# Kernel optimization log

Measured on AMD Instinct MI355X. Metric: run time of the kernel, lower is better.

## Reference

```python
import jax, jax.numpy as jnp
import numpy as np

B, K, C, NCLS = 4096, 20, 512, 8631


def setup_inputs() -> dict:
    key = jax.random.key(0)
    k0, k1, k2, k3 = jax.random.split(key, 4)
    x = jax.random.normal(k0, (B * K, C), dtype=jnp.float32)
    # NAN pooling (torch.cat of [1,C,K] tensors) requires uniform set lengths
    lst_lens = jnp.full((B,), K, dtype=jnp.int32)
    # learned params (torch init zeros them out, which degenerates the math to
    # mean pooling; use small random values for a meaningful correctness baseline)
    q = jax.random.normal(k1, (C,), dtype=jnp.float32) * 0.02        # NAN_Attention.q
    W_att = jax.random.normal(k2, (C, C), dtype=jnp.float32) * 0.02  # attention fc
    b_att = jnp.zeros((C,), dtype=jnp.float32)
    W_fc = jax.random.normal(k3, (NCLS, C), dtype=jnp.float32) * 0.02  # classifier
    b_fc = jnp.zeros((NCLS,), dtype=jnp.float32)
    return {"x": x, "lst_lens": lst_lens, "q": q, "W_att": W_att,
            "b_att": b_att, "W_fc": W_fc, "b_fc": b_fc}


def reference(x, lst_lens, q, W_att, b_att, W_fc, b_fc):
    eps = 1e-12
    # F.normalize: L2 normalize each row
    xn = x / jnp.maximum(jnp.linalg.norm(x, axis=1, keepdims=True), eps)
    nset = lst_lens.shape[0]
    k = xn.shape[0] // nset              # uniform set length (required by NAN cat)
    xs = xn.reshape(nset, k, -1)         # [B, K, C]  (== Xs.transpose of [B,C,K])

    # pass 1: global query q -> attention-weighted mean r
    s1 = jax.nn.softmax(jnp.einsum('c,bkc->bk', q, xs), axis=-1)   # [B, K]
    r = jnp.einsum('bk,bkc->bc', s1, xs)                            # [B, C]

    # pass 2: adapted query new_q = tanh(fc(r))
    new_q = jnp.tanh(r @ W_att.T + b_att)                           # [B, C]
    s2 = jax.nn.softmax(jnp.einsum('bc,bkc->bk', new_q, xs), axis=-1)
    feats = jnp.einsum('bk,bkc->bc', s2, xs)                        # [B, C]

    logits = feats @ W_fc.T + b_fc                                  # [B, NCLS]
    return feats, logits
```

## Files before the change

kernel.cpp:

```cpp
#include <hip/hip_runtime.h>
#include <math.h>

#define BB   4096
#define KK   20
#define CC   512
#define NCLS 8631
#define NPAD 8704
#define KSP  1536

typedef __attribute__((ext_vector_type(8))) short bf16x8;
typedef __attribute__((ext_vector_type(4))) float f32x4;

static __device__ __forceinline__ unsigned short f2bf(float f) {
    unsigned int u = __float_as_uint(f);
    u += 0x7FFFu + ((u >> 16) & 1u);
    return (unsigned short)(u >> 16);
}
static __device__ __forceinline__ float bf2f(unsigned short h) {
    return __uint_as_float(((unsigned int)h) << 16);
}

__global__ __launch_bounds__(320) void pool_kernel(
    const float* __restrict__ x,
    const float* __restrict__ qbase, size_t q_stride,
    float* __restrict__ outv)
{
    __shared__ float xs[KK][CC];
    __shared__ float red[KK];
    __shared__ float dots[KK];

    const int b   = blockIdx.x;
    const int tid = threadIdx.x;

    const float4* src = (const float4*)(x + (size_t)b * (KK * CC));
    float4* dst = (float4*)&xs[0][0];
    #pragma unroll
    for (int i = tid; i < KK * CC / 4; i += 320) dst[i] = src[i];

    const float* qv = qbase + (size_t)b * q_stride;
    __syncthreads();

    const int g = tid >> 4;
    const int l = tid & 15;
    float ss = 0.f, qd = 0.f;
    for (int c = l; c < CC; c += 16) {
        float v = xs[g][c];
        ss = fmaf(v, v, ss);
        qd = fmaf(qv[c], v, qd);
    }
    #pragma unroll
    for (int m = 8; m >= 1; m >>= 1) {
        ss += __shfl_xor(ss, m);
        qd += __shfl_xor(qd, m);
    }
    if (l == 0) {
        float inv = 1.f / fmaxf(sqrtf(ss), 1e-12f);
        red[g]  = inv;
        dots[g] = qd * inv;
    }
    __syncthreads();

    if (tid < KK) {
        float m = -1e30f;
        #pragma unroll
        for (int k = 0; k < KK; ++k) m = fmaxf(m, dots[k]);
        float s = 0.f;
        #pragma unroll
        for (int k = 0; k < KK; ++k) s += __expf(dots[k] - m);
        float w = __expf(dots[tid] - m) / s;
        red[tid] = w * red[tid];
    }
    __syncthreads();

    float* ob = outv + (size_t)b * CC;
    for (int c = tid; c < CC; c += 320) {
        float acc = 0.f;
        #pragma unroll
        for (int k = 0; k < KK; ++k) acc = fmaf(red[k], xs[k][c], acc);
        ob[c] = acc;
    }
}

template<int BM, int BN, int BK, int TM, int TN, bool TANH>
__global__ __launch_bounds__(256) void gemm_bt(
    const float* __restrict__ A,
    const float* __restrict__ Bt,
    const float* __restrict__ bias,
    float* __restrict__ Cmat,
    int M, int N, int Kd)
{
    constexpr int NT = (BM / TM) * (BN / TN);
    static_assert(NT == 256, "256 threads expected");
    static_assert(BM * BK == NT * 4 && BN * BK == NT * 4, "one float4 per thread per tile");

    __shared__ float As[BK][BM];
    __shared__ float Bs[BK][BN];

    const int tid = threadIdx.x;
    const int m0 = blockIdx.x * BM;
    const int n0 = blockIdx.y * BN;
    constexpr int TX = BN / TN;
    const int tx = tid % TX;
    const int ty = tid / TX;

    constexpr int KV = BK / 4;
    const int lr = tid / KV;
    const int lc = (tid % KV) * 4;

    float acc[TM][TN] = {};

    for (int k0 = 0; k0 < Kd; k0 += BK) {
        float4 av = *(const float4*)&A[(size_t)(m0 + lr) * Kd + k0 + lc];
        float4 bv = make_float4(0.f, 0.f, 0.f, 0.f);
        int nrow = n0 + lr;
        if (nrow < N) bv = *(const float4*)&Bt[(size_t)nrow * Kd + k0 + lc];

        __syncthreads();
        As[lc + 0][lr] = av.x; As[lc + 1][lr] = av.y;
        As[lc + 2][lr] = av.z; As[lc + 3][lr] = av.w;
        Bs[lc + 0][lr] = bv.x; Bs[lc + 1][lr] = bv.y;
        Bs[lc + 2][lr] = bv.z; Bs[lc + 3][lr] = bv.w;
        __syncthreads();

        #pragma unroll
        for (int kk = 0; kk < BK; ++kk) {
            float a[TM], bb[TN];
            #pragma unroll
            for (int u = 0; u < TM; u += 4)
                *(float4*)&a[u] = *(const float4*)&As[kk][ty * TM + u];
            #pragma unroll
            for (int u = 0; u < TN; u += 4)
                *(float4*)&bb[u] = *(const float4*)&Bs[kk][tx * TN + u];
            #pragma unroll
            for (int i = 0; i < TM; ++i)
                #pragma unroll
                for (int j = 0; j < TN; ++j)
                    acc[i][j] = fmaf(a[i], bb[j], acc[i][j]);
        }
    }

    #pragma unroll
    for (int i = 0; i < TM; ++i) {
        int m = m0 + ty * TM + i;
        #pragma unroll
        for (int j = 0; j < TN; ++j) {
            int n = n0 + tx * TN + j;
            if (n < N) {
                float v = acc[i][j] + bias[n];
                if (TANH) v = tanhf(v);
                Cmat[(size_t)m * N + n] = v;
            }
        }
    }
}

template<int L0, int L1, int L2>
__global__ __launch_bounds__(256) void conv_split(
    const float* __restrict__ in, unsigned short* __restrict__ out,
    int rows_in, int rows_out)
{
    int idx = blockIdx.x * 256 + threadIdx.x;
    int row = idx >> 7;
    if (row >= rows_out) return;
    int c4 = (idx & 127) << 2;

    float4 v = make_float4(0.f, 0.f, 0.f, 0.f);
    if (row < rows_in) v = *(const float4*)&in[(size_t)row * CC + c4];

    unsigned short h0 = f2bf(v.x), h1 = f2bf(v.y), h2 = f2bf(v.z), h3 = f2bf(v.w);
    ushort4 hv = make_ushort4(h0, h1, h2, h3);
    ushort4 lv = make_ushort4(f2bf(v.x - bf2f(h0)), f2bf(v.y - bf2f(h1)),
                              f2bf(v.z - bf2f(h2)), f2bf(v.w - bf2f(h3)));

    unsigned short* o = out + (size_t)row * KSP + c4;
    *(ushort4*)(o)          = L0 ? lv : hv;
    *(ushort4*)(o + CC)     = L1 ? lv : hv;
    *(ushort4*)(o + 2 * CC) = L2 ? lv : hv;
}

__global__ __launch_bounds__(256) void gemm_mfma_bt(
    const unsigned short* __restrict__ A,
    const unsigned short* __restrict__ B,
    const float* __restrict__ bias,
    float* __restrict__ Cmat,
    int Nn)
{
    __shared__ unsigned short As[128][32];
    __shared__ unsigned short Bs[128][32];

    const int tid  = threadIdx.x;
    const int lane = tid & 63;
    const int w    = tid >> 6;
    const int m0   = blockIdx.x * 128;
    const int n0   = blockIdx.y * 128;
    const int wr   = w >> 1;
    const int wc   = w & 1;

    f32x4 acc[4][4] = {};

    const int chunk0 = w * 128;

    for (int k0 = 0; k0 < KSP; k0 += 32) {
        __syncthreads();
        #pragma unroll
        for (int j = 0; j < 2; ++j) {
            const int cbase = chunk0 + j * 64;
            const int ch    = cbase + lane;
            const int row   = ch >> 2;
            const int kcol  = (ch & 3) << 3;
            const unsigned short* ga = A + (size_t)(m0 + row) * KSP + k0 + kcol;
            __builtin_amdgcn_global_load_lds(
                (const __attribute__((address_space(1))) void*)ga,
                (__attribute__((address_space(3))) void*)((char*)&As[0][0] + cbase * 16),
                16, 0, 0);
            const unsigned short* gb = B + (size_t)(n0 + row) * KSP + k0 + kcol;
            __builtin_amdgcn_global_load_lds(
                (const __attribute__((address_space(1))) void*)gb,
                (__attribute__((address_space(3))) void*)((char*)&Bs[0][0] + cbase * 16),
                16, 0, 0);
        }
        __syncthreads();

        const int kk = (lane >> 4) << 3;
        const int rl = lane & 15;
        bf16x8 af[4], bfr[4];
        #pragma unroll
        for (int i = 0; i < 4; ++i)
            af[i] = *(const bf16x8*)&As[wr * 64 + i * 16 + rl][kk];
        #pragma unroll
        for (int j = 0; j < 4; ++j)
            bfr[j] = *(const bf16x8*)&Bs[wc * 64 + j * 16 + rl][kk];

        #pragma unroll
        for (int i = 0; i < 4; ++i)
            #pragma unroll
            for (int j = 0; j < 4; ++j)
                acc[i][j] = __builtin_amdgcn_mfma_f32_16x16x32_bf16(
                    af[i], bfr[j], acc[i][j], 0, 0, 0);
    }

    const int rowb = m0 + wr * 64 + ((lane >> 4) << 2);
    const int colb = n0 + wc * 64 + (lane & 15);
    #pragma unroll
    for (int j = 0; j < 4; ++j) {
        const int n = colb + j * 16;
        if (n < Nn) {
            const float bia = bias[n];
            #pragma unroll
            for (int i = 0; i < 4; ++i) {
                #pragma unroll
                for (int r = 0; r < 4; ++r) {
                    const int m = rowb + i * 16 + r;
                    Cmat[(size_t)m * Nn + n] = acc[i][j][r] + bia;
                }
            }
        }
    }
}

extern "C" void kernel_launch(void* const* d_in, const int* in_sizes, int n_in,
                              void* d_out, int out_size, void* d_ws, size_t ws_size,
                              hipStream_t stream)
{
    const float* x     = (const float*)d_in[0];
    const float* q     = (const float*)d_in[2];
    const float* W_att = (const float*)d_in[3];
    const float* b_att = (const float*)d_in[4];
    const float* W_fc  = (const float*)d_in[5];
    const float* b_fc  = (const float*)d_in[6];

    float* feats  = (float*)d_out;
    float* logits = feats + (size_t)BB * CC;

    float* r_buf  = logits;
    float* nq_buf = logits + (size_t)BB * CC;

    const size_t needA = (size_t)BB * KSP * sizeof(unsigned short);
    const size_t needB = (size_t)NPAD * KSP * sizeof(unsigned short);
    const bool use_mfma = ws_size >= needA + needB;
    unsigned short* Abuf = (unsigned short*)d_ws;
    unsigned short* Bbuf = Abuf + (size_t)BB * KSP;

    pool_kernel<<<BB, 320, 0, stream>>>(x, q, (size_t)0, r_buf);

    gemm_bt<64, 64, 16, 4, 4, true><<<dim3(BB / 64, CC / 64), 256, 0, stream>>>(
        r_buf, W_att, b_att, nq_buf, BB, CC, CC);

    pool_kernel<<<BB, 320, 0, stream>>>(x, nq_buf, (size_t)CC, feats);

    if (use_mfma) {
        conv_split<0, 0, 1><<<(NPAD * (CC / 4)) / 256, 256, 0, stream>>>(
            W_fc, Bbuf, NCLS, NPAD);
        conv_split<0, 1, 0><<<(BB * (CC / 4)) / 256, 256, 0, stream>>>(
            feats, Abuf, BB, BB);
        gemm_mfma_bt<<<dim3(BB / 128, NPAD / 128), 256, 0, stream>>>(
            Abuf, Bbuf, b_fc, logits, NCLS);
    } else {
        gemm_bt<128, 128, 8, 8, 8, false><<<dim3(BB / 128, (NCLS + 127) / 128), 256, 0, stream>>>(
            feats, W_fc, b_fc, logits, BB, NCLS, CC);
    }
}
```

Measured before the change: 654.4 us.

## Add 256x256 pipelined MFMA classifier GEMM, MFMA attention GEMM, vectorized pooling

Replaces the 128x128 classifier GEMM with a 256x256-tile, 512-thread kernel that uses a 4-slot LDS ring fed by direct global-to-LDS loads, a swizzled LDS layout, XCD-aware block remapping and setprio around the MFMA bursts. The attention fc GEMM moves from the FP32 SIMT kernel to the split-bf16 MFMA path with tanh fused into its epilogue, which adds conversion kernels and workspace. The pooling kernel is vectorized to float4 LDS reads and stores. Together these target the large classifier GEMM and the scalar attention GEMM, at the cost of more workspace, high LDS use per block, and a more complex synchronization scheme.

```diff
diff --git a/kernel.cpp b/kernel.cpp
--- a/kernel.cpp
+++ b/kernel.cpp
@@ -7,6 +7,7 @@
 #define NCLS 8631
 #define NPAD 8704
 #define KSP  1536
+#define NTK  48
 
 typedef __attribute__((ext_vector_type(8))) short bf16x8;
 typedef __attribute__((ext_vector_type(4))) float f32x4;
@@ -34,7 +35,6 @@
 
     const float4* src = (const float4*)(x + (size_t)b * (KK * CC));
     float4* dst = (float4*)&xs[0][0];
-    #pragma unroll
     for (int i = tid; i < KK * CC / 4; i += 320) dst[i] = src[i];
 
     const float* qv = qbase + (size_t)b * q_stride;
@@ -43,10 +43,14 @@
     const int g = tid >> 4;
     const int l = tid & 15;
     float ss = 0.f, qd = 0.f;
-    for (int c = l; c < CC; c += 16) {
-        float v = xs[g][c];
-        ss = fmaf(v, v, ss);
-        qd = fmaf(qv[c], v, qd);
+    #pragma unroll
+    for (int c = 0; c < CC; c += 64) {
+        float4 v  = *(const float4*)&xs[g][c + l * 4];
+        float4 q4 = *(const float4*)&qv[c + l * 4];
+        ss = fmaf(v.x, v.x, ss); ss = fmaf(v.y, v.y, ss);
+        ss = fmaf(v.z, v.z, ss); ss = fmaf(v.w, v.w, ss);
+        qd = fmaf(q4.x, v.x, qd); qd = fmaf(q4.y, v.y, qd);
+        qd = fmaf(q4.z, v.z, qd); qd = fmaf(q4.w, v.w, qd);
     }
     #pragma unroll
     for (int m = 8; m >= 1; m >>= 1) {
@@ -73,11 +77,16 @@
     __syncthreads();
 
     float* ob = outv + (size_t)b * CC;
-    for (int c = tid; c < CC; c += 320) {
-        float acc = 0.f;
-        #pragma unroll
-        for (int k = 0; k < KK; ++k) acc = fmaf(red[k], xs[k][c], acc);
-        ob[c] = acc;
+    for (int c = tid * 4; c < CC; c += 1280) {
+        float4 a = make_float4(0.f, 0.f, 0.f, 0.f);
+        #pragma unroll
+        for (int k = 0; k < KK; ++k) {
+            float w = red[k];
+            float4 v = *(const float4*)&xs[k][c];
+            a.x = fmaf(w, v.x, a.x); a.y = fmaf(w, v.y, a.y);
+            a.z = fmaf(w, v.z, a.z); a.w = fmaf(w, v.w, a.w);
+        }
+        *(float4*)&ob[c] = a;
     }
 }
 
@@ -91,8 +100,6 @@
 {
     constexpr int NT = (BM / TM) * (BN / TN);
     static_assert(NT == 256, "256 threads expected");
-    static_assert(BM * BK == NT * 4 && BN * BK == NT * 4, "one float4 per thread per tile");
-
     __shared__ float As[BK][BM];
     __shared__ float Bs[BK][BN];
 
@@ -102,7 +109,6 @@
     constexpr int TX = BN / TN;
     const int tx = tid % TX;
     const int ty = tid / TX;
-
     constexpr int KV = BK / 4;
     const int lr = tid / KV;
     const int lc = (tid % KV) * 4;
@@ -114,14 +120,12 @@
         float4 bv = make_float4(0.f, 0.f, 0.f, 0.f);
         int nrow = n0 + lr;
         if (nrow < N) bv = *(const float4*)&Bt[(size_t)nrow * Kd + k0 + lc];
-
         __syncthreads();
         As[lc + 0][lr] = av.x; As[lc + 1][lr] = av.y;
         As[lc + 2][lr] = av.z; As[lc + 3][lr] = av.w;
         Bs[lc + 0][lr] = bv.x; Bs[lc + 1][lr] = bv.y;
         Bs[lc + 2][lr] = bv.z; Bs[lc + 3][lr] = bv.w;
         __syncthreads();
-
         #pragma unroll
         for (int kk = 0; kk < BK; ++kk) {
             float a[TM], bb[TN];
@@ -138,7 +142,6 @@
                     acc[i][j] = fmaf(a[i], bb[j], acc[i][j]);
         }
     }
-
     #pragma unroll
     for (int i = 0; i < TM; ++i) {
         int m = m0 + ty * TM + i;
@@ -178,6 +181,7 @@
     *(ushort4*)(o + 2 * CC) = L2 ? lv : hv;
 }
 
+template<bool TANH>
 __global__ __launch_bounds__(256) void gemm_mfma_bt(
     const unsigned short* __restrict__ A,
     const unsigned short* __restrict__ B,
@@ -197,7 +201,6 @@
     const int wc   = w & 1;
 
     f32x4 acc[4][4] = {};
-
     const int chunk0 = w * 128;
 
     for (int k0 = 0; k0 < KSP; k0 += 32) {
@@ -251,11 +254,142 @@
                 #pragma unroll
                 for (int r = 0; r < 4; ++r) {
                     const int m = rowb + i * 16 + r;
-                    Cmat[(size_t)m * Nn + n] = acc[i][j][r] + bia;
+                    float v = acc[i][j][r] + bia;
+                    if (TANH) v = tanhf(v);
+                    Cmat[(size_t)m * Nn + n] = v;
                 }
             }
         }
     }
+}
+
+__global__ __launch_bounds__(512, 2) void gemm_mfma256(
+    const unsigned short* __restrict__ A,
+    const unsigned short* __restrict__ B,
+    const float* __restrict__ bias,
+    float* __restrict__ Cmat,
+    int Nn, int mblocks)
+{
+    __shared__ char smem[131072];
+
+    const int tid  = threadIdx.x;
+    const int lane = tid & 63;
+    const int w    = tid >> 6;
+    const int wm   = w >> 2;
+    const int wn   = w & 3;
+    const int rl   = lane & 15;
+    const int cw   = lane >> 4;
+
+    const int cpx = (int)gridDim.x >> 3;
+    const int wg  = ((int)blockIdx.x & 7) * cpx + ((int)blockIdx.x >> 3);
+    const int m0  = (wg % mblocks) * 256;
+    const int n0  = (wg / mblocks) * 256;
+
+    const int rowA = tid >> 2;
+    const int lcs  = (tid & 3) ^ ((rowA >> 1) & 3);
+    const unsigned short* pA0 = A + (size_t)(m0 + rowA) * KSP + lcs * 8;
+    const unsigned short* pA1 = pA0 + (size_t)128 * KSP;
+    const unsigned short* pB0 = B + (size_t)(n0 + rowA) * KSP + lcs * 8;
+    const unsigned short* pB1 = pB0 + (size_t)128 * KSP;
+    const int wbyte = w * 1024;
+
+    #define STAGE_A(slot, k0s)                                                  \
+        do {                                                                    \
+            __builtin_amdgcn_global_load_lds(                                   \
+                (const __attribute__((address_space(1))) void*)(pA0 + (k0s)),   \
+                (__attribute__((address_space(3))) void*)(smem + (slot) * 16384 + wbyte), \
+                16, 0, 0);                                                      \
+            __builtin_amdgcn_global_load_lds(                                   \
+                (const __attribute__((address_space(1))) void*)(pA1 + (k0s)),   \
+                (__attribute__((address_space(3))) void*)(smem + (slot) * 16384 + 8192 + wbyte), \
+                16, 0, 0);                                                      \
+        } while (0)
+    #define STAGE_B(slot, k0s)                                                  \
+        do {                                                                    \
+            __builtin_amdgcn_global_load_lds(                                   \
+                (const __attribute__((address_space(1))) void*)(pB0 + (k0s)),   \
+                (__attribute__((address_space(3))) void*)(smem + 65536 + (slot) * 16384 + wbyte), \
+                16, 0, 0);                                                      \
+            __builtin_amdgcn_global_load_lds(                                   \
+                (const __attribute__((address_space(1))) void*)(pB1 + (k0s)),   \
+                (__attribute__((address_space(3))) void*)(smem + 65536 + (slot) * 16384 + 8192 + wbyte), \
+                16, 0, 0);                                                      \
+        } while (0)
+
+    const int albase = rl * 64 + ((cw ^ ((rl >> 1) & 3)) << 4);
+
+    f32x4 acc[8][4] = {};
+
+    #pragma unroll
+    for (int pt = 0; pt < 3; ++pt) {
+        STAGE_A(pt, pt * 32);
+        STAGE_B(pt, pt * 32);
+    }
+    asm volatile("s_waitcnt vmcnt(8)" ::: "memory");
+    __builtin_amdgcn_s_barrier();
+
+    for (int t = 0; t < NTK; ++t) {
+        const int slot = t & 3;
+        const int ts   = t + 3;
+        const int k0s  = (ts < NTK) ? ts * 32 : 0;
+        const int sst  = ts & 3;
+        const char* sa = smem + slot * 16384 + wm * 8192 + albase;
+        const char* sb = smem + 65536 + slot * 16384 + wn * 4096 + albase;
+
+        bf16x8 af[4], bf[4];
+        #pragma unroll
+        for (int i = 0; i < 4; ++i) af[i] = *(const bf16x8*)(sa + i * 1024);
+        #pragma unroll
+        for (int n = 0; n < 4; ++n) bf[n] = *(const bf16x8*)(sb + n * 1024);
+        STAGE_A(sst, k0s);
+        __builtin_amdgcn_s_barrier();
+        asm volatile("s_waitcnt lgkmcnt(0)" ::: "memory");
+        __builtin_amdgcn_s_setprio(1);
+        #pragma unroll
+        for (int i = 0; i < 4; ++i)
+            #pragma unroll
+            for (int n = 0; n < 4; ++n)
+                acc[i][n] = __builtin_amdgcn_mfma_f32_16x16x32_bf16(
+                    af[i], bf[n], acc[i][n], 0, 0, 0);
+        __builtin_amdgcn_s_setprio(0);
+        __builtin_amdgcn_s_barrier();
+
+        #pragma unroll
+        for (int i = 0; i < 4; ++i) af[i] = *(const bf16x8*)(sa + 4096 + i * 1024);
+        STAGE_B(sst, k0s);
+        __builtin_amdgcn_s_barrier();
+        asm volatile("s_waitcnt lgkmcnt(0)" ::: "memory");
+        __builtin_amdgcn_s_setprio(1);
+        #pragma unroll
+        for (int i = 0; i < 4; ++i)
+            #pragma unroll
+            for (int n = 0; n < 4; ++n)
+                acc[4 + i][n] = __builtin_amdgcn_mfma_f32_16x16x32_bf16(
+                    af[i], bf[n], acc[4 + i][n], 0, 0, 0);
+        __builtin_amdgcn_s_setprio(0);
+        asm volatile("s_waitcnt vmcnt(8)" ::: "memory");
+        __builtin_amdgcn_s_barrier();
+    }
+    asm volatile("s_waitcnt vmcnt(0)" ::: "memory");
+
+    const int mwb = m0 + wm * 128 + (cw << 2);
+    const int nwb = n0 + wn * 64 + rl;
+    #pragma unroll
+    for (int mf = 0; mf < 8; ++mf) {
+        #pragma unroll
+        for (int n = 0; n < 4; ++n) {
+            const int ncol = nwb + n * 16;
+            if (ncol < Nn) {
+                const float bia = bias[ncol];
+                float* cp = Cmat + (size_t)(mwb + mf * 16) * Nn + ncol;
+                #pragma unroll
+                for (int r = 0; r < 4; ++r)
+                    cp[(size_t)r * Nn] = acc[mf][n][r] + bia;
+            }
+        }
+    }
+    #undef STAGE_A
+    #undef STAGE_B
 }
 
 extern "C" void kernel_launch(void* const* d_in, const int* in_sizes, int n_in,
@@ -275,26 +409,42 @@
     float* r_buf  = logits;
     float* nq_buf = logits + (size_t)BB * CC;
 
-    const size_t needA = (size_t)BB * KSP * sizeof(unsigned short);
-    const size_t needB = (size_t)NPAD * KSP * sizeof(unsigned short);
-    const bool use_mfma = ws_size >= needA + needB;
+    const size_t need_cls = (size_t)(BB + NPAD) * KSP * 2;
+    const size_t need_all = need_cls + (size_t)(BB + CC) * KSP * 2;
+    const bool mfma_cls = ws_size >= need_cls;
+    const bool mfma_att = ws_size >= need_all;
+
     unsigned short* Abuf = (unsigned short*)d_ws;
     unsigned short* Bbuf = Abuf + (size_t)BB * KSP;
-
-    pool_kernel<<<BB, 320, 0, stream>>>(x, q, (size_t)0, r_buf);
-
-    gemm_bt<64, 64, 16, 4, 4, true><<<dim3(BB / 64, CC / 64), 256, 0, stream>>>(
-        r_buf, W_att, b_att, nq_buf, BB, CC, CC);
-
-    pool_kernel<<<BB, 320, 0, stream>>>(x, nq_buf, (size_t)CC, feats);
-
-    if (use_mfma) {
+    unsigned short* Arb  = Bbuf + (size_t)NPAD * KSP;
+    unsigned short* Wab  = Arb  + (size_t)BB * KSP;
+
+    if (mfma_cls)
         conv_split<0, 0, 1><<<(NPAD * (CC / 4)) / 256, 256, 0, stream>>>(
             W_fc, Bbuf, NCLS, NPAD);
+    if (mfma_att)
+        conv_split<0, 0, 1><<<(CC * (CC / 4)) / 256, 256, 0, stream>>>(
+            W_att, Wab, CC, CC);
+
+    pool_kernel<<<BB, 320, 0, stream>>>(x, q, (size_t)0, r_buf);
+
+    if (mfma_att) {
+        conv_split<0, 1, 0><<<(BB * (CC / 4)) / 256, 256, 0, stream>>>(
+            r_buf, Arb, BB, BB);
+        gemm_mfma_bt<true><<<dim3(BB / 128, CC / 128), 256, 0, stream>>>(
+            Arb, Wab, b_att, nq_buf, CC);
+    } else {
+        gemm_bt<64, 64, 16, 4, 4, true><<<dim3(BB / 64, CC / 64), 256, 0, stream>>>(
+            r_buf, W_att, b_att, nq_buf, BB, CC, CC);
+    }
+
+    pool_kernel<<<BB, 320, 0, stream>>>(x, nq_buf, (size_t)CC, feats);
+
+    if (mfma_cls) {
         conv_split<0, 1, 0><<<(BB * (CC / 4)) / 256, 256, 0, stream>>>(
             feats, Abuf, BB, BB);
-        gemm_mfma_bt<<<dim3(BB / 128, NPAD / 128), 256, 0, stream>>>(
-            Abuf, Bbuf, b_fc, logits, NCLS);
+        gemm_mfma256<<<dim3((BB / 256) * (NPAD / 256)), 512, 0, stream>>>(
+            Abuf, Bbuf, b_fc, logits, NCLS, BB / 256);
     } else {
         gemm_bt<128, 128, 8, 8, 8, false><<<dim3(BB / 128, (NCLS + 127) / 128), 256, 0, stream>>>(
             feats, W_fc, b_fc, logits, BB, NCLS, CC);
```

Result: faster. 532.9 us (-18.6%).
